# Kernel optimization log

Hardware: AMD Instinct MI355X
Metric: run time of the kernel (lower is better)

Reference implementation:

```python
import jax, jax.numpy as jnp
import numpy as np

N_QUBITS = 4
N_LAYERS = 2
PROJ_DIM = 64
B = 262144
C64 = jnp.complex64


def setup_inputs() -> dict:
    key = jax.random.key(0)
    ks = jax.random.split(key, 4)
    x = jax.random.normal(ks[0], (B, N_QUBITS), dtype=jnp.float32)
    # TorchLayer default init: uniform(0, 2*pi)
    weights = jax.random.uniform(ks[1], (N_LAYERS, N_QUBITS, 3), dtype=jnp.float32) * (2.0 * np.pi)
    W = jax.random.normal(ks[2], (PROJ_DIM, N_QUBITS), dtype=jnp.float32) * 0.5
    b = jnp.zeros((PROJ_DIM,), dtype=jnp.float32)
    gamma = jnp.ones((PROJ_DIM,), dtype=jnp.float32)
    beta = jnp.zeros((PROJ_DIM,), dtype=jnp.float32)
    return {"x": x, "weights": weights, "W": W, "b": b, "gamma": gamma, "beta": beta}


def _apply_1q(state, U, w):
    # state: (B, 2,2,2,2); U: (2,2) shared or (B,2,2) per-sample
    s = jnp.moveaxis(state, 1 + w, -1)
    if U.ndim == 3:
        s = jnp.einsum('b...j,bij->b...i', s, U)
    else:
        s = s @ U.T
    return jnp.moveaxis(s, -1, 1 + w)


def _apply_cnot(state, c, t):
    s = jnp.moveaxis(state, (1 + c, 1 + t), (-2, -1))
    s = jnp.concatenate([s[..., :1, :], s[..., 1:, ::-1]], axis=-2)
    return jnp.moveaxis(s, (-2, -1), (1 + c, 1 + t))


def _rot_matrix(phi, theta, omega):
    # PennyLane Rot = RZ(omega) @ RY(theta) @ RZ(phi)
    c = jnp.cos(theta / 2).astype(C64)
    s = jnp.sin(theta / 2).astype(C64)
    ep = jnp.exp(-0.5j * (phi + omega).astype(C64))
    em = jnp.exp(0.5j * (phi - omega).astype(C64))
    return jnp.array(0, C64) + jnp.stack([
        jnp.stack([ep * c, -em * s]),
        jnp.stack([jnp.conj(em) * s, jnp.conj(ep) * c])], axis=0)


def _circuit(angles, weights):
    # angles: (B, n) real; returns (B, n) PauliZ expvals
    n = N_QUBITS
    Bn = angles.shape[0]
    state = jnp.zeros((Bn, 2 ** n), dtype=C64).at[:, 0].set(1.0)
    state = state.reshape((Bn,) + (2,) * n)
    # AngleEmbedding: RX(angle_w) on wire w (per-sample angles)
    half = angles / 2
    cos_h = jnp.cos(half).astype(C64)
    isin_h = (-1j) * jnp.sin(half).astype(C64)
    for w in range(n):
        U = jnp.stack([jnp.stack([cos_h[:, w], isin_h[:, w]], -1),
                       jnp.stack([isin_h[:, w], cos_h[:, w]], -1)], -2)  # (B,2,2)
        state = _apply_1q(state, U, w)
    # StronglyEntanglingLayers: Rot on each wire, then CNOT ring with range r
    for l in range(N_LAYERS):
        for w in range(n):
            U = _rot_matrix(weights[l, w, 0], weights[l, w, 1], weights[l, w, 2])
            state = _apply_1q(state, U, w)
        r = l % (n - 1) + 1
        for w in range(n):
            state = _apply_cnot(state, w, (w + r) % n)
    probs = jnp.abs(state) ** 2  # (B,2,...,2)
    sign = jnp.array([1.0, -1.0], dtype=jnp.float32)
    zs = []
    for w in range(n):
        axes = tuple(a for a in range(1, n + 1) if a != 1 + w)
        zs.append(probs.sum(axis=axes) @ sign)
    return jnp.stack(zs, -1)  # (B, n)


def reference(x, weights, W, b, gamma, beta):
    angles = jnp.tanh(x) * np.pi
    q = _circuit(angles, weights)            # (B, n_qubits)
    q = jax.nn.softmax(q, axis=-1)
    h = q @ W.T + b                          # (B, proj_dim)
    mu = h.mean(axis=-1, keepdims=True)
    var = ((h - mu) ** 2).mean(axis=-1, keepdims=True)
    hn = (h - mu) * jax.lax.rsqrt(var + 1e-5)
    return hn * gamma + beta
```

## Files before the change

### kernel.cpp

```cpp
#include <hip/hip_runtime.h>
#include <cstdint>


#define WS_VRT 0
#define WS_VIT 256
#define WS_A   512
#define WS_B0  768
#define WS_G   832
#define WS_g   848
#define WS_C0  852
#define WREG   864

__global__ __launch_bounds__(256) void qb_fused(const float* __restrict__ x,
                                                const float* __restrict__ wts,
                                                const float* __restrict__ W,
                                                const float* __restrict__ bias,
                                                const float* __restrict__ gamma,
                                                const float* __restrict__ beta,
                                                float* __restrict__ out) {
    __shared__ __align__(16) float wlds[WREG];
    const int tid  = threadIdx.x;
    const int wv   = tid >> 6;
    const int lane = tid & 63;

    const int sample = blockIdx.x * 256 + tid;
    const float4 xv = ((const float4*)x)[sample];

    const int k4t = lane & 15;
    const float4 Bt4v = ((const float4*)beta)[k4t];

    float m[16];
    {
        const float xa[4] = {xv.x, xv.y, xv.z, xv.w};
        float c4[4], s4[4];
        #pragma unroll
        for (int w = 0; w < 4; ++w) {
            const float h = tanhf(xa[w]) * 1.5707963267948966f;
            __sincosf(h, &s4[w], &c4[w]);
        }
        const float e01[4] = {c4[0]*c4[1], c4[0]*s4[1], s4[0]*c4[1], s4[0]*s4[1]};
        const float e23[4] = {c4[2]*c4[3], c4[2]*s4[3], s4[2]*c4[3], s4[2]*s4[3]};
        #pragma unroll
        for (int j = 0; j < 16; ++j) m[j] = e01[j>>2]*e23[j&3];
    }

    if (wv == 0) {
        const int row = lane >> 2;
        const int cg  = lane & 3;
        float ur[4], ui[4];
        #pragma unroll
        for (int c = 0; c < 4; ++c) { ur[c] = (row == 4*cg + c) ? 1.f : 0.f; ui[c] = 0.f; }

        #pragma unroll
        for (int l = 0; l < 2; ++l) {
            #pragma unroll
            for (int w = 0; w < 4; ++w) {
                const float ph = wts[l*12 + w*3 + 0];
                const float th = wts[l*12 + w*3 + 1];
                const float om = wts[l*12 + w*3 + 2];
                float st, ct; __sincosf(0.5f*th, &st, &ct);
                float sp, cp; __sincosf(0.5f*(ph+om), &sp, &cp);
                float sm, cm; __sincosf(0.5f*(ph-om), &sm, &cm);
                const float a00r =  cp*ct, a00i = -sp*ct;
                const float a01r = -cm*st, a01i = -sm*st;
                const float a10r =  cm*st, a10i = -sm*st;
                const float a11r =  cp*ct, a11i =  sp*ct;
                const int m8 = 8 >> w;
                const int xm = m8 << 2;
                const bool hi = (row & m8) != 0;
                #pragma unroll
                for (int c = 0; c < 4; ++c) {
                    const float pr = __shfl_xor(ur[c], xm, 64);
                    const float pi = __shfl_xor(ui[c], xm, 64);
                    float nr, ni;
                    if (!hi) {
                        nr = a00r*ur[c] - a00i*ui[c] + a01r*pr - a01i*pi;
                        ni = a00r*ui[c] + a00i*ur[c] + a01r*pi + a01i*pr;
                    } else {
                        nr = a11r*ur[c] - a11i*ui[c] + a10r*pr - a10i*pi;
                        ni = a11r*ui[c] + a11i*ur[c] + a10r*pi + a10i*pr;
                    }
                    ur[c] = nr; ui[c] = ni;
                }
            }
            const int rr = (l == 0) ? 1 : 2;
            #pragma unroll
            for (int w = 0; w < 4; ++w) {
                const int cmk = 8 >> w;
                const int tmk = 8 >> ((w + rr) & 3);
                const int src = (row & cmk) ? (row ^ tmk) : row;
                const int srcLane = src*4 + cg;
                #pragma unroll
                for (int c = 0; c < 4; ++c) {
                    ur[c] = __shfl(ur[c], srcLane, 64);
                    ui[c] = __shfl(ui[c], srcLane, 64);
                }
            }
        }

        #pragma unroll
        for (int c = 0; c < 4; ++c) {
            const int col = 4*cg + c;
            const int p = __popc(col) & 3;
            float vr, vi;
            if (p == 0)      { vr =  ur[c]; vi =  ui[c]; }
            else if (p == 1) { vr =  ui[c]; vi = -ur[c]; }
            else if (p == 2) { vr = -ur[c]; vi = -ui[c]; }
            else             { vr = -ui[c]; vi =  ur[c]; }
            wlds[WS_VRT + col*16 + row] = vr;
            wlds[WS_VIT + col*16 + row] = vi;
        }

        {
            const int k = lane;
            const float4 wk = ((const float4*)W)[k];
            const float w0 = wk.x, w1 = wk.y, w2 = wk.z, w3 = wk.w;
            const float bk = bias[k];
            auto wsum = [](float v) {
                #pragma unroll
                for (int o = 32; o; o >>= 1) v += __shfl_xor(v, o, 64);
                return v;
            };
            const float inv64 = 1.f/64.f;
            const float m0 = wsum(w0)*inv64, m1 = wsum(w1)*inv64;
            const float m2 = wsum(w2)*inv64, m3 = wsum(w3)*inv64;
            const float bm = wsum(bk)*inv64;
            float cc[4] = {w0-m0, w1-m1, w2-m2, w3-m3};
            const float bc = bk - bm;
            const float gk = gamma[k];
            float4 av;
            av.x = cc[0]*gk; av.y = cc[1]*gk; av.z = cc[2]*gk; av.w = cc[3]*gk;
            ((float4*)(wlds + WS_A))[k] = av;
            wlds[WS_B0 + k] = bc*gk;
            #pragma unroll
            for (int a = 0; a < 4; ++a)
                #pragma unroll
                for (int b2 = a; b2 < 4; ++b2) {
                    const float s = wsum(cc[a]*cc[b2])*inv64;
                    if (k == 0) {
                        wlds[WS_G + a*4 + b2] = s;
                        wlds[WS_G + b2*4 + a] = s;
                    }
                }
            #pragma unroll
            for (int a = 0; a < 4; ++a) {
                const float s = wsum(bc*cc[a])*inv64;
                if (k == 0) wlds[WS_g + a] = s;
            }
            { const float s = wsum(bc*bc)*inv64; if (k == 0) wlds[WS_C0] = s; }
        }
    }

    __syncthreads();

    float r[16], si[16];
    #pragma unroll
    for (int i = 0; i < 16; ++i) { r[i] = 0.f; si[i] = 0.f; }
    const float4* vr4 = (const float4*)(wlds + WS_VRT);
    const float4* vi4 = (const float4*)(wlds + WS_VIT);
    #pragma unroll
    for (int j = 0; j < 16; ++j) {
        const float mj = m[j];
        #pragma unroll
        for (int i4 = 0; i4 < 4; ++i4) {
            const float4 a = vr4[j*4 + i4];
            const float4 b = vi4[j*4 + i4];
            r [i4*4+0] = fmaf(a.x, mj, r [i4*4+0]);
            r [i4*4+1] = fmaf(a.y, mj, r [i4*4+1]);
            r [i4*4+2] = fmaf(a.z, mj, r [i4*4+2]);
            r [i4*4+3] = fmaf(a.w, mj, r [i4*4+3]);
            si[i4*4+0] = fmaf(b.x, mj, si[i4*4+0]);
            si[i4*4+1] = fmaf(b.y, mj, si[i4*4+1]);
            si[i4*4+2] = fmaf(b.z, mj, si[i4*4+2]);
            si[i4*4+3] = fmaf(b.w, mj, si[i4*4+3]);
        }
    }
    float z0 = 0.f, z1 = 0.f, z2 = 0.f, z3 = 0.f;
    #pragma unroll
    for (int i = 0; i < 16; ++i) {
        const float p = r[i]*r[i] + si[i]*si[i];
        z0 += (i & 8) ? -p : p;
        z1 += (i & 4) ? -p : p;
        z2 += (i & 2) ? -p : p;
        z3 += (i & 1) ? -p : p;
    }
    const float mx = fmaxf(fmaxf(z0, z1), fmaxf(z2, z3));
    const float e0 = __expf(z0-mx), e1 = __expf(z1-mx);
    const float e2 = __expf(z2-mx), e3 = __expf(z3-mx);
    const float rs = 1.f / (e0+e1+e2+e3);
    const float qx = e0*rs, qy = e1*rs, qz = e2*rs, qw = e3*rs;

    float var = wlds[WS_C0];
    {
        const float4 Gs0 = ((const float4*)(wlds + WS_G))[0];
        const float4 Gs1 = ((const float4*)(wlds + WS_G))[1];
        const float4 Gs2 = ((const float4*)(wlds + WS_G))[2];
        const float4 Gs3 = ((const float4*)(wlds + WS_G))[3];
        const float4 gv  = ((const float4*)(wlds + WS_g))[0];
        const float qa[4] = {qx, qy, qz, qw};
        const float4 Gs[4] = {Gs0, Gs1, Gs2, Gs3};
        const float ga[4] = {gv.x, gv.y, gv.z, gv.w};
        #pragma unroll
        for (int a = 0; a < 4; ++a) {
            float t = 2.f * ga[a];
            t = fmaf(Gs[a].x, qa[0], t);
            t = fmaf(Gs[a].y, qa[1], t);
            t = fmaf(Gs[a].z, qa[2], t);
            t = fmaf(Gs[a].w, qa[3], t);
            var = fmaf(qa[a], t, var);
        }
    }
    const float inv = rsqrtf(var + 1e-5f);

    float4 A4[4];
    #pragma unroll
    for (int u = 0; u < 4; ++u) A4[u] = ((const float4*)(wlds + WS_A))[k4t*4 + u];
    const float4 B04v = ((const float4*)(wlds + WS_B0))[k4t];
    const float B04[4] = {B04v.x, B04v.y, B04v.z, B04v.w};
    const float Bt4[4] = {Bt4v.x, Bt4v.y, Bt4v.z, Bt4v.w};

    float4* outv = (float4*)out + (size_t)blockIdx.x * 4096 + wv * 1024;
    #pragma unroll
    for (int iter = 0; iter < 16; ++iter) {
        const int src = iter*4 + (lane >> 4);
        const float bqx = __shfl(qx,  src, 64);
        const float bqy = __shfl(qy,  src, 64);
        const float bqz = __shfl(qz,  src, 64);
        const float bqw = __shfl(qw,  src, 64);
        const float biv = __shfl(inv, src, 64);
        float4 o;
        float* op = (float*)&o;
        #pragma unroll
        for (int u = 0; u < 4; ++u) {
            float t = B04[u];
            t = fmaf(A4[u].x, bqx, t);
            t = fmaf(A4[u].y, bqy, t);
            t = fmaf(A4[u].z, bqz, t);
            t = fmaf(A4[u].w, bqw, t);
            op[u] = fmaf(t, biv, Bt4[u]);
        }
        outv[iter*64 + lane] = o;
    }
}

extern "C" void kernel_launch(void* const* d_in, const int* in_sizes, int n_in,
                              void* d_out, int out_size, void* d_ws, size_t ws_size,
                              hipStream_t stream) {
    const float* x     = (const float*)d_in[0];
    const float* wts   = (const float*)d_in[1];
    const float* W     = (const float*)d_in[2];
    const float* bias  = (const float*)d_in[3];
    const float* gamma = (const float*)d_in[4];
    const float* beta  = (const float*)d_in[5];
    float* out = (float*)d_out;
    const int B = in_sizes[0] / 4;

    hipLaunchKernelGGL(qb_fused, dim3(B / 256), dim3(256), 0, stream,
                       x, wts, W, bias, gamma, beta, out);
}
```

Baseline: 95.06 us.

## Split LN-weight prep onto second wave and broadcast q via LDS instead of shuffles

Moves the W/bias/gamma statistics computation from wave 0 into wave 1, so it runs in parallel with wave 0's circuit-matrix construction. In the output loop, per-sample softmax results and inverse std are staged in shared memory and read back as broadcast loads, replacing five cross-lane shuffles per iteration. Adds a minimum-blocks occupancy hint to launch bounds. LDS use grows to about 8.5 KB per block, and the extra LDS traffic may compete with the output stores.

Result: faster. 92.51 us (-2.7%).

```diff
diff --git a/kernel.cpp b/kernel.cpp
--- a/kernel.cpp
+++ b/kernel.cpp
@@ -9,15 +9,17 @@
 #define WS_G   832
 #define WS_g   848
 #define WS_C0  852
-#define WREG   864
-
-__global__ __launch_bounds__(256) void qb_fused(const float* __restrict__ x,
-                                                const float* __restrict__ wts,
-                                                const float* __restrict__ W,
-                                                const float* __restrict__ bias,
-                                                const float* __restrict__ gamma,
-                                                const float* __restrict__ beta,
-                                                float* __restrict__ out) {
+#define WS_Q   864
+#define WS_INV 1888
+#define WREG   2144
+
+__global__ __launch_bounds__(256, 4) void qb_fused(const float* __restrict__ x,
+                                                   const float* __restrict__ wts,
+                                                   const float* __restrict__ W,
+                                                   const float* __restrict__ bias,
+                                                   const float* __restrict__ gamma,
+                                                   const float* __restrict__ beta,
+                                                   float* __restrict__ out) {
     __shared__ __align__(16) float wlds[WREG];
     const int tid  = threadIdx.x;
     const int wv   = tid >> 6;
@@ -110,45 +112,43 @@
             wlds[WS_VRT + col*16 + row] = vr;
             wlds[WS_VIT + col*16 + row] = vi;
         }
-
-        {
-            const int k = lane;
-            const float4 wk = ((const float4*)W)[k];
-            const float w0 = wk.x, w1 = wk.y, w2 = wk.z, w3 = wk.w;
-            const float bk = bias[k];
-            auto wsum = [](float v) {
-                #pragma unroll
-                for (int o = 32; o; o >>= 1) v += __shfl_xor(v, o, 64);
-                return v;
-            };
-            const float inv64 = 1.f/64.f;
-            const float m0 = wsum(w0)*inv64, m1 = wsum(w1)*inv64;
-            const float m2 = wsum(w2)*inv64, m3 = wsum(w3)*inv64;
-            const float bm = wsum(bk)*inv64;
-            float cc[4] = {w0-m0, w1-m1, w2-m2, w3-m3};
-            const float bc = bk - bm;
-            const float gk = gamma[k];
-            float4 av;
-            av.x = cc[0]*gk; av.y = cc[1]*gk; av.z = cc[2]*gk; av.w = cc[3]*gk;
-            ((float4*)(wlds + WS_A))[k] = av;
-            wlds[WS_B0 + k] = bc*gk;
-            #pragma unroll
-            for (int a = 0; a < 4; ++a)
-                #pragma unroll
-                for (int b2 = a; b2 < 4; ++b2) {
-                    const float s = wsum(cc[a]*cc[b2])*inv64;
-                    if (k == 0) {
-                        wlds[WS_G + a*4 + b2] = s;
-                        wlds[WS_G + b2*4 + a] = s;
-                    }
+    } else if (wv == 1) {
+        const int k = lane;
+        const float4 wk = ((const float4*)W)[k];
+        const float w0 = wk.x, w1 = wk.y, w2 = wk.z, w3 = wk.w;
+        const float bk = bias[k];
+        auto wsum = [](float v) {
+            #pragma unroll
+            for (int o = 32; o; o >>= 1) v += __shfl_xor(v, o, 64);
+            return v;
+        };
+        const float inv64 = 1.f/64.f;
+        const float m0 = wsum(w0)*inv64, m1 = wsum(w1)*inv64;
+        const float m2 = wsum(w2)*inv64, m3 = wsum(w3)*inv64;
+        const float bm = wsum(bk)*inv64;
+        float cc[4] = {w0-m0, w1-m1, w2-m2, w3-m3};
+        const float bc = bk - bm;
+        const float gk = gamma[k];
+        float4 av;
+        av.x = cc[0]*gk; av.y = cc[1]*gk; av.z = cc[2]*gk; av.w = cc[3]*gk;
+        ((float4*)(wlds + WS_A))[k] = av;
+        wlds[WS_B0 + k] = bc*gk;
+        #pragma unroll
+        for (int a = 0; a < 4; ++a)
+            #pragma unroll
+            for (int b2 = a; b2 < 4; ++b2) {
+                const float s = wsum(cc[a]*cc[b2])*inv64;
+                if (k == 0) {
+                    wlds[WS_G + a*4 + b2] = s;
+                    wlds[WS_G + b2*4 + a] = s;
                 }
-            #pragma unroll
-            for (int a = 0; a < 4; ++a) {
-                const float s = wsum(bc*cc[a])*inv64;
-                if (k == 0) wlds[WS_g + a] = s;
             }
-            { const float s = wsum(bc*bc)*inv64; if (k == 0) wlds[WS_C0] = s; }
-        }
+        #pragma unroll
+        for (int a = 0; a < 4; ++a) {
+            const float s = wsum(bc*cc[a])*inv64;
+            if (k == 0) wlds[WS_g + a] = s;
+        }
+        { const float s = wsum(bc*bc)*inv64; if (k == 0) wlds[WS_C0] = s; }
     }
 
     __syncthreads();
@@ -212,6 +212,9 @@
     }
     const float inv = rsqrtf(var + 1e-5f);
 
+    ((float4*)(wlds + WS_Q))[wv*64 + lane] = make_float4(qx, qy, qz, qw);
+    wlds[WS_INV + wv*64 + lane] = inv;
+
     float4 A4[4];
     #pragma unroll
     for (int u = 0; u < 4; ++u) A4[u] = ((const float4*)(wlds + WS_A))[k4t*4 + u];
@@ -219,27 +222,25 @@
     const float B04[4] = {B04v.x, B04v.y, B04v.z, B04v.w};
     const float Bt4[4] = {Bt4v.x, Bt4v.y, Bt4v.z, Bt4v.w};
 
-    float4* outv = (float4*)out + (size_t)blockIdx.x * 4096 + wv * 1024;
+    float4* outv = (float4*)out + (size_t)blockIdx.x * 4096 + wv * 1024 + lane;
+    const float4* qld = (const float4*)(wlds + WS_Q) + wv*64 + (lane >> 4);
+    const float*  ild = wlds + WS_INV + wv*64 + (lane >> 4);
     #pragma unroll
     for (int iter = 0; iter < 16; ++iter) {
-        const int src = iter*4 + (lane >> 4);
-        const float bqx = __shfl(qx,  src, 64);
-        const float bqy = __shfl(qy,  src, 64);
-        const float bqz = __shfl(qz,  src, 64);
-        const float bqw = __shfl(qw,  src, 64);
-        const float biv = __shfl(inv, src, 64);
+        const float4 q  = qld[iter*4];
+        const float  iv = ild[iter*4];
         float4 o;
         float* op = (float*)&o;
         #pragma unroll
         for (int u = 0; u < 4; ++u) {
             float t = B04[u];
-            t = fmaf(A4[u].x, bqx, t);
-            t = fmaf(A4[u].y, bqy, t);
-            t = fmaf(A4[u].z, bqz, t);
-            t = fmaf(A4[u].w, bqw, t);
-            op[u] = fmaf(t, biv, Bt4[u]);
-        }
-        outv[iter*64 + lane] = o;
+            t = fmaf(A4[u].x, q.x, t);
+            t = fmaf(A4[u].y, q.y, t);
+            t = fmaf(A4[u].z, q.z, t);
+            t = fmaf(A4[u].w, q.w, t);
+            op[u] = fmaf(t, iv, Bt4[u]);
+        }
+        outv[iter*64] = o;
     }
 }
 
```
